# Kernel tuning notes

Measured on AMD Instinct MI355X. Metric: run time of the kernel, lower is better.

The kernel has to match this reference:

```python
import jax, jax.numpy as jnp
import numpy as np
from jax import lax

B, CIN, H, W = 32, 256, 28, 28
COUT, KS, KEXP = 256, 3, 4
HIDDEN = int(CIN * 0.25)  # ratio hard-coded to 0.25 in the module


def setup_inputs() -> dict:
    key = jax.random.key(0)
    k1, k2, k3, k4 = jax.random.split(key, 4)
    x = jax.random.normal(k1, (B, CIN, H, W), dtype=jnp.float32)
    # SE (InvertedEx) params: fc1 (1x1 conv, no bias), fc2 (1x1 conv, bias)
    fc1_w = jax.random.normal(k2, (HIDDEN, CIN), dtype=jnp.float32) * np.float32(np.sqrt(2.0 / CIN))
    fc2_w = jax.random.normal(k3, (KEXP * COUT, HIDDEN), dtype=jnp.float32) * np.float32(np.sqrt(2.0 / HIDDEN))
    fc2_b = jnp.zeros((KEXP * COUT,), dtype=jnp.float32)
    # K expert conv kernels, he_std = sqrt(2) * (CIN*KS^2)^-0.5
    he_std = np.float32(np.sqrt(2.0) * (CIN * KS * KS) ** -0.5)
    weight = jax.random.normal(k4, (KEXP, COUT, CIN, KS, KS), dtype=jnp.float32) * he_std
    return {"x": x, "fc1_w": fc1_w, "fc2_w": fc2_w, "fc2_b": fc2_b, "weight": weight}


def reference(x, fc1_w, fc2_w, fc2_b, weight):
    # --- SE routing ---
    pooled = jnp.mean(x, axis=(2, 3))                        # [B, CIN]
    h = jax.nn.relu(pooled @ fc1_w.T)                        # [B, HIDDEN]
    y = (h @ fc2_w.T + fc2_b).reshape(B, KEXP, COUT)         # [B, K, COUT]
    prob = jax.nn.softmax(y / jnp.sqrt(jnp.float32(HIDDEN)), axis=1)  # softmax over K
    # --- aggregate per-sample kernels ---
    agg_w = jnp.einsum('bko,koihw->boihw', prob, weight)     # [B, COUT, CIN, KS, KS]
    # --- per-sample conv (batched implicit GEMM via vmap) ---
    def conv1(xi, wi):
        return lax.conv_general_dilated(
            xi[None], wi, window_strides=(1, 1), padding=((1, 1), (1, 1)),
            dimension_numbers=('NCHW', 'OIHW', 'NCHW'))[0]
    out = jax.vmap(conv1)(x, agg_w)                          # [B, COUT, H, W]
    return out
```

## Files before the change

### kernel.cpp

```cpp
#include <hip/hip_runtime.h>
#include <math.h>

#define B_    32
#define CIN_  256
#define HW_   784
#define H_    28
#define W_    28
#define COUT_ 256
#define KEXP_ 4
#define HID_  64

typedef short short8 __attribute__((ext_vector_type(8)));
typedef float floatx16 __attribute__((ext_vector_type(16)));

__device__ __forceinline__ unsigned short f2bf(float f) {
    union { float f; unsigned int u; } v; v.f = f;
    unsigned int r = (v.u + 0x7FFFu + ((v.u >> 16) & 1u)) >> 16;
    return (unsigned short)r;
}

__global__ __launch_bounds__(256) void xpose_pool_kernel(const float* __restrict__ x,
                                                         unsigned short* __restrict__ x_t,
                                                         float* __restrict__ pooled) {
    __shared__ float tile[32][33];
    int bid = blockIdx.x;
    int b   = bid / 200;
    int rem = bid - b * 200;
    int ic0 = (rem / 25) * 32;
    int px0 = (rem % 25) * 32;
    int t = threadIdx.x;
    int c = t & 31, rr = t >> 5;
    #pragma unroll
    for (int r = 0; r < 4; ++r) {
        int icr = rr + r * 8;
        int px = px0 + c;
        float v = (px < HW_) ? x[((size_t)(b * CIN_ + ic0 + icr)) * HW_ + px] : 0.f;
        tile[icr][c] = v;
    }
    __syncthreads();
    #pragma unroll
    for (int r = 0; r < 4; ++r) {
        int pxr = rr + r * 8;
        int px = px0 + pxr;
        if (px < HW_)
            x_t[((size_t)b * HW_ + px) * CIN_ + ic0 + c] = f2bf(tile[c][pxr]);
    }
    if (t < 32) {
        float s = 0.f;
        #pragma unroll
        for (int cc = 0; cc < 32; ++cc) s += tile[t][cc];
        atomicAdd(&pooled[b * CIN_ + ic0 + t], s * (1.0f / HW_));
    }
}

__global__ __launch_bounds__(256) void pool_kernel(const float* __restrict__ x,
                                                   float* __restrict__ pooled) {
    int w = blockIdx.x * 4 + (threadIdx.x >> 6);
    int lane = threadIdx.x & 63;
    const float* p = x + (size_t)w * HW_;
    float s = 0.f;
    for (int i = lane; i < HW_; i += 64) s += p[i];
    for (int off = 32; off; off >>= 1) s += __shfl_down(s, off);
    if (lane == 0) pooled[w] = s * (1.0f / HW_);
}

__global__ __launch_bounds__(256) void se2_kernel(const float* __restrict__ pooled,
                                                  const float* __restrict__ fc1_w,
                                                  const float* __restrict__ fc2_w,
                                                  const float* __restrict__ fc2_b,
                                                  float* __restrict__ prob) {
    __shared__ float pl[CIN_];
    __shared__ float h[HID_];
    __shared__ float wb[16640];
    int b = blockIdx.x, t = threadIdx.x;
    pl[t] = pooled[b * CIN_ + t];
    #pragma unroll
    for (int i = 0; i < 16; ++i) {
        int l = t + i * 256;
        float4 v = *(const float4*)(fc1_w + (size_t)l * 4);
        int r = l >> 6, cc = (l & 63) * 4;
        float* dst = &wb[r * 257 + cc];
        dst[0] = v.x; dst[1] = v.y; dst[2] = v.z; dst[3] = v.w;
    }
    __syncthreads();
    if (t < HID_) {
        float s = 0.f;
        const float* wr = &wb[t * 257];
        for (int c = 0; c < CIN_; ++c) s += pl[c] * wr[c];
        h[t] = fmaxf(s, 0.f);
    }
    float yk[KEXP_];
    for (int k = 0; k < KEXP_; ++k) {
        __syncthreads();
        #pragma unroll
        for (int i = 0; i < 16; ++i) {
            int l = t + i * 256;
            float4 v = *(const float4*)(fc2_w + (size_t)k * COUT_ * HID_ + (size_t)l * 4);
            int o = l >> 4, jj = (l & 15) * 4;
            float* dst = &wb[o * 65 + jj];
            dst[0] = v.x; dst[1] = v.y; dst[2] = v.z; dst[3] = v.w;
        }
        __syncthreads();
        float s = fc2_b[k * COUT_ + t];
        const float* wr = &wb[t * 65];
        #pragma unroll
        for (int j = 0; j < HID_; ++j) s += h[j] * wr[j];
        yk[k] = s * 0.125f;
    }
    float m = yk[0];
    for (int k = 1; k < KEXP_; ++k) m = fmaxf(m, yk[k]);
    float e[KEXP_], sum = 0.f;
    for (int k = 0; k < KEXP_; ++k) { e[k] = expf(yk[k] - m); sum += e[k]; }
    float inv = 1.0f / sum;
    for (int k = 0; k < KEXP_; ++k)
        prob[b * (KEXP_ * COUT_) + k * COUT_ + t] = e[k] * inv;
}

__global__ __launch_bounds__(256) void agg2_kernel(const float* __restrict__ weight,
                                                   const float* __restrict__ prob,
                                                   unsigned short* __restrict__ agg) {
    __shared__ float ws_w[KEXP_ * CIN_ * 9];
    __shared__ float pb[KEXP_][8];
    int bid = blockIdx.x;
    int oc = bid & 255;
    int b0 = (bid >> 8) * 8;
    int t = threadIdx.x;
    for (int e = t; e < KEXP_ * CIN_ * 9; e += 256) {
        int k = e / (CIN_ * 9);
        int r = e - k * (CIN_ * 9);
        ws_w[e] = weight[((size_t)(k * COUT_ + oc)) * (CIN_ * 9) + r];
    }
    if (t < KEXP_ * 8) {
        int k = t >> 3, bb = t & 7;
        pb[k][bb] = prob[(b0 + bb) * (KEXP_ * COUT_) + k * COUT_ + oc];
    }
    __syncthreads();
    int ic = t;
    for (int rs = 0; rs < 9; ++rs) {
        float w0 = ws_w[0 * CIN_ * 9 + ic * 9 + rs];
        float w1 = ws_w[1 * CIN_ * 9 + ic * 9 + rs];
        float w2 = ws_w[2 * CIN_ * 9 + ic * 9 + rs];
        float w3 = ws_w[3 * CIN_ * 9 + ic * 9 + rs];
        #pragma unroll
        for (int bb = 0; bb < 8; ++bb) {
            float s = pb[0][bb] * w0 + pb[1][bb] * w1 + pb[2][bb] * w2 + pb[3][bb] * w3;
            agg[(((size_t)(b0 + bb) * 9 + rs) * COUT_ + oc) * CIN_ + ic] = f2bf(s);
        }
    }
}

__global__ __launch_bounds__(256, 2) void conv_mfma2_kernel(const unsigned short* __restrict__ x_t,
                                                            const unsigned short* __restrict__ agg,
                                                            float* __restrict__ out) {
    __shared__ __align__(16) short Xs[6 * 35 * 72];
    __shared__ __align__(16) short As[2][128 * 72];

    int gid = blockIdx.x;
    int rowblk = gid >> 6;
    int pair = gid & 63;
    int b = pair >> 1;
    int oc0 = (pair & 1) * 128;
    int py0 = rowblk * 4;

    int t = threadIdx.x;
    int lane = t & 63, w = t >> 6;
    int ml = lane & 31, kh = lane >> 5;

    floatx16 acc[4];
    #pragma unroll
    for (int j = 0; j < 4; ++j)
        #pragma unroll
        for (int r = 0; r < 16; ++r) acc[j][r] = 0.f;

    const unsigned short* xtb = x_t + (size_t)b * HW_ * CIN_;
    const unsigned short* agb = agg + ((size_t)b * 9 * COUT_ + oc0) * CIN_;

    int arow = t >> 3, ag = t & 7;

    for (int ic0 = 0; ic0 < CIN_; ic0 += 64) {
        #pragma unroll
        for (int i = 0; i < 7; ++i) {
            int l = t + i * 256;
            if (l < 6 * 35 * 8) {
                int pos = l >> 3, g = l & 7;
                int row = pos / 35, col = pos - row * 35;
                int gy = py0 - 1 + row, gx = col - 1;
                short8 v = (short8)0;
                if ((unsigned)gy < 28u && (unsigned)gx < 28u)
                    v = *(const short8*)(xtb + ((size_t)(gy * W_ + gx)) * CIN_ + ic0 + g * 8);
                *(short8*)&Xs[pos * 72 + g * 8] = v;
            }
        }
        {
            const unsigned short* ap = agb + ic0 + (size_t)ag * 8;
            #pragma unroll
            for (int i = 0; i < 4; ++i) {
                short8 v = *(const short8*)(ap + (size_t)(arow + i * 32) * CIN_);
                *(short8*)&As[0][(arow + i * 32) * 72 + ag * 8] = v;
            }
        }
        __syncthreads();

        for (int rs = 0; rs < 9; ++rs) {
            int cur = rs & 1;
            int dy = rs / 3, dx = rs - dy * 3;
            short8 rv0, rv1, rv2, rv3;
            if (rs < 8) {
                const unsigned short* ap = agb + (size_t)(rs + 1) * COUT_ * CIN_ + ic0 + (size_t)ag * 8;
                rv0 = *(const short8*)(ap + (size_t)(arow +  0) * CIN_);
                rv1 = *(const short8*)(ap + (size_t)(arow + 32) * CIN_);
                rv2 = *(const short8*)(ap + (size_t)(arow + 64) * CIN_);
                rv3 = *(const short8*)(ap + (size_t)(arow + 96) * CIN_);
            }
            #pragma unroll
            for (int kk = 0; kk < 4; ++kk) {
                short8 a = *(const short8*)&As[cur][(w * 32 + ml) * 72 + kk * 16 + kh * 8];
                #pragma unroll
                for (int j = 0; j < 4; ++j) {
                    short8 bf = *(const short8*)&Xs[((j + dy) * 35 + (ml + dx)) * 72 + kk * 16 + kh * 8];
                    acc[j] = __builtin_amdgcn_mfma_f32_32x32x16_bf16(a, bf, acc[j], 0, 0, 0);
                }
            }
            if (rs < 8) {
                short* dst = &As[cur ^ 1][arow * 72 + ag * 8];
                *(short8*)(dst +  0 * 72)      = rv0;
                *(short8*)(dst + 32 * 72)      = rv1;
                *(short8*)(dst + 64 * 72)      = rv2;
                *(short8*)(dst + 96 * 72)      = rv3;
            }
            __syncthreads();
        }
    }

    int col = ml;
    if (col < W_) {
        #pragma unroll
        for (int j = 0; j < 4; ++j) {
            int y = py0 + j;
            #pragma unroll
            for (int r = 0; r < 16; ++r) {
                int ocg = oc0 + w * 32 + (r & 3) + 8 * (r >> 2) + 4 * kh;
                out[((size_t)(b * COUT_ + ocg)) * HW_ + y * W_ + col] = acc[j][r];
            }
        }
    }
}

__global__ __launch_bounds__(256) void conv_kernel(const float* __restrict__ x,
                                                   const float* __restrict__ weight,
                                                   const float* __restrict__ prob,
                                                   float* __restrict__ out) {
    __shared__ float xs[30 * 30];
    __shared__ float wagg[8][32][12];
    __shared__ float pl[KEXP_][8];

    int b  = blockIdx.x >> 5;
    int o0 = (blockIdx.x & 31) * 8;
    int t  = threadIdx.x;

    if (t < 32) {
        int k = t >> 3, oc = t & 7;
        pl[k][oc] = prob[b * (KEXP_ * COUT_) + k * COUT_ + o0 + oc];
    }
    int p0 = t;
    int pr[4], pc[4];
    bool pv[4];
    #pragma unroll
    for (int j = 0; j < 4; ++j) {
        int p = p0 + j * 256;
        pv[j] = p < HW_;
        pr[j] = p / W_;
        pc[j] = p % W_;
    }
    float acc[8][4];
    #pragma unroll
    for (int oc = 0; oc < 8; ++oc)
        #pragma unroll
        for (int j = 0; j < 4; ++j) acc[oc][j] = 0.f;

    int aoc = t >> 5, aii = t & 31;

    for (int ic0 = 0; ic0 < CIN_; ic0 += 32) {
        __syncthreads();
        {
            float w9[9];
            #pragma unroll
            for (int j = 0; j < 9; ++j) w9[j] = 0.f;
            int i = ic0 + aii;
            #pragma unroll
            for (int k = 0; k < KEXP_; ++k) {
                float pk = pl[k][aoc];
                const float* wp = weight + ((size_t)(k * COUT_ + o0 + aoc) * CIN_ + i) * 9;
                #pragma unroll
                for (int j = 0; j < 9; ++j) w9[j] += pk * wp[j];
            }
            #pragma unroll
            for (int j = 0; j < 9; ++j) wagg[aoc][aii][j] = w9[j];
        }
        for (int ii = 0; ii < 32; ++ii) {
            int i = ic0 + ii;
            __syncthreads();
            const float* xp = x + (size_t)(b * CIN_ + i) * HW_;
            for (int e = t; e < 900; e += 256) {
                int ry = e / 30, cx = e - ry * 30;
                int gy = ry - 1, gx = cx - 1;
                float v = 0.f;
                if ((unsigned)gy < 28u && (unsigned)gx < 28u) v = xp[gy * W_ + gx];
                xs[e] = v;
            }
            __syncthreads();
            float xv[4][9];
            #pragma unroll
            for (int j = 0; j < 4; ++j) {
                if (pv[j]) {
                    const float* xr = &xs[pr[j] * 30 + pc[j]];
                    xv[j][0] = xr[0];  xv[j][1] = xr[1];  xv[j][2] = xr[2];
                    xv[j][3] = xr[30]; xv[j][4] = xr[31]; xv[j][5] = xr[32];
                    xv[j][6] = xr[60]; xv[j][7] = xr[61]; xv[j][8] = xr[62];
                } else {
                    #pragma unroll
                    for (int q = 0; q < 9; ++q) xv[j][q] = 0.f;
                }
            }
            #pragma unroll
            for (int oc = 0; oc < 8; ++oc) {
                float4 wa = *(const float4*)&wagg[oc][ii][0];
                float4 wb2 = *(const float4*)&wagg[oc][ii][4];
                float  wc = wagg[oc][ii][8];
                #pragma unroll
                for (int j = 0; j < 4; ++j) {
                    acc[oc][j] += xv[j][0] * wa.x + xv[j][1] * wa.y + xv[j][2] * wa.z
                                + xv[j][3] * wa.w + xv[j][4] * wb2.x + xv[j][5] * wb2.y
                                + xv[j][6] * wb2.z + xv[j][7] * wb2.w + xv[j][8] * wc;
                }
            }
        }
    }
    #pragma unroll
    for (int oc = 0; oc < 8; ++oc) {
        float* op = out + (size_t)(b * COUT_ + o0 + oc) * HW_ + p0;
        #pragma unroll
        for (int j = 0; j < 4; ++j)
            if (pv[j]) op[j * 256] = acc[oc][j];
    }
}

extern "C" void kernel_launch(void* const* d_in, const int* in_sizes, int n_in,
                              void* d_out, int out_size, void* d_ws, size_t ws_size,
                              hipStream_t stream) {
    const float* x     = (const float*)d_in[0];
    const float* fc1_w = (const float*)d_in[1];
    const float* fc2_w = (const float*)d_in[2];
    const float* fc2_b = (const float*)d_in[3];
    const float* weight= (const float*)d_in[4];
    float* out = (float*)d_out;

    char* ws = (char*)d_ws;
    float* pooled = (float*)(ws);
    float* prob   = (float*)(ws + 32768);
    unsigned short* x_t = (unsigned short*)(ws + 163840);
    unsigned short* agg = (unsigned short*)(ws + 13008896);
    const size_t WS_NEED = 50757632;

    if (ws_size >= WS_NEED) {
        hipMemsetAsync(pooled, 0, B_ * CIN_ * sizeof(float), stream);
        xpose_pool_kernel<<<B_ * 8 * 25, 256, 0, stream>>>(x, x_t, pooled);
        se2_kernel<<<B_, 256, 0, stream>>>(pooled, fc1_w, fc2_w, fc2_b, prob);
        agg2_kernel<<<4 * COUT_, 256, 0, stream>>>(weight, prob, agg);
        conv_mfma2_kernel<<<7 * 64, 256, 0, stream>>>(x_t, agg, out);
    } else {
        pool_kernel<<<(B_ * CIN_) / 4, 256, 0, stream>>>(x, pooled);
        se2_kernel<<<B_, 256, 0, stream>>>(pooled, fc1_w, fc2_w, fc2_b, prob);
        conv_kernel<<<B_ * (COUT_ / 8), 256, 0, stream>>>(x, weight, prob, out);
    }
}
```

Before: 156.8 us.

## Rework dynamic-conv pipeline: partial pooling, vectorized aggregation, register-streamed conv tiles

Swaps the pooled atomics and memset for per-tile partial sums that the SE kernel reduces itself, so one launch and the atomic traffic go away. Vectorizes the weight aggregation with float4 loads and packed 4-wide bf16 stores. Rewrites the MFMA conv to compute 7 output rows per block, with each A fragment reused across three row offsets. A fragments are prefetched straight from global into registers rather than staged in LDS, and X is double-buffered across input-channel chunks. Launching 256 blocks at one block per CU leaves occupancy low and raises register pressure, and the partial buffer aliases the agg region.

```diff
diff --git a/kernel.cpp b/kernel.cpp
--- a/kernel.cpp
+++ b/kernel.cpp
@@ -11,6 +11,7 @@
 #define HID_  64
 
 typedef short short8 __attribute__((ext_vector_type(8)));
+typedef unsigned short ushort4v __attribute__((ext_vector_type(4)));
 typedef float floatx16 __attribute__((ext_vector_type(16)));
 
 __device__ __forceinline__ unsigned short f2bf(float f) {
@@ -21,13 +22,15 @@
 
 __global__ __launch_bounds__(256) void xpose_pool_kernel(const float* __restrict__ x,
                                                          unsigned short* __restrict__ x_t,
-                                                         float* __restrict__ pooled) {
+                                                         float* __restrict__ partial) {
     __shared__ float tile[32][33];
     int bid = blockIdx.x;
     int b   = bid / 200;
     int rem = bid - b * 200;
-    int ic0 = (rem / 25) * 32;
-    int px0 = (rem % 25) * 32;
+    int icg = rem / 25;
+    int pxt = rem % 25;
+    int ic0 = icg * 32;
+    int px0 = pxt * 32;
     int t = threadIdx.x;
     int c = t & 31, rr = t >> 5;
     #pragma unroll
@@ -49,7 +52,7 @@
         float s = 0.f;
         #pragma unroll
         for (int cc = 0; cc < 32; ++cc) s += tile[t][cc];
-        atomicAdd(&pooled[b * CIN_ + ic0 + t], s * (1.0f / HW_));
+        partial[((size_t)b * 25 + pxt) * CIN_ + ic0 + t] = s * (1.0f / HW_);
     }
 }
 
@@ -62,6 +65,63 @@
     for (int i = lane; i < HW_; i += 64) s += p[i];
     for (int off = 32; off; off >>= 1) s += __shfl_down(s, off);
     if (lane == 0) pooled[w] = s * (1.0f / HW_);
+}
+
+__global__ __launch_bounds__(256) void se3_kernel(const float* __restrict__ partial,
+                                                  const float* __restrict__ fc1_w,
+                                                  const float* __restrict__ fc2_w,
+                                                  const float* __restrict__ fc2_b,
+                                                  float* __restrict__ prob) {
+    __shared__ float pl[CIN_];
+    __shared__ float h[HID_];
+    __shared__ float wb[16640];
+    int b = blockIdx.x, t = threadIdx.x;
+    {
+        float s = 0.f;
+        for (int pt = 0; pt < 25; ++pt)
+            s += partial[((size_t)b * 25 + pt) * CIN_ + t];
+        pl[t] = s;
+    }
+    #pragma unroll
+    for (int i = 0; i < 16; ++i) {
+        int l = t + i * 256;
+        float4 v = *(const float4*)(fc1_w + (size_t)l * 4);
+        int r = l >> 6, cc = (l & 63) * 4;
+        float* dst = &wb[r * 257 + cc];
+        dst[0] = v.x; dst[1] = v.y; dst[2] = v.z; dst[3] = v.w;
+    }
+    __syncthreads();
+    if (t < HID_) {
+        float s = 0.f;
+        const float* wr = &wb[t * 257];
+        for (int c = 0; c < CIN_; ++c) s += pl[c] * wr[c];
+        h[t] = fmaxf(s, 0.f);
+    }
+    float yk[KEXP_];
+    for (int k = 0; k < KEXP_; ++k) {
+        __syncthreads();
+        #pragma unroll
+        for (int i = 0; i < 16; ++i) {
+            int l = t + i * 256;
+            float4 v = *(const float4*)(fc2_w + (size_t)k * COUT_ * HID_ + (size_t)l * 4);
+            int o = l >> 4, jj = (l & 15) * 4;
+            float* dst = &wb[o * 65 + jj];
+            dst[0] = v.x; dst[1] = v.y; dst[2] = v.z; dst[3] = v.w;
+        }
+        __syncthreads();
+        float s = fc2_b[k * COUT_ + t];
+        const float* wr = &wb[t * 65];
+        #pragma unroll
+        for (int j = 0; j < HID_; ++j) s += h[j] * wr[j];
+        yk[k] = s * 0.125f;
+    }
+    float m = yk[0];
+    for (int k = 1; k < KEXP_; ++k) m = fmaxf(m, yk[k]);
+    float e[KEXP_], sum = 0.f;
+    for (int k = 0; k < KEXP_; ++k) { e[k] = expf(yk[k] - m); sum += e[k]; }
+    float inv = 1.0f / sum;
+    for (int k = 0; k < KEXP_; ++k)
+        prob[b * (KEXP_ * COUT_) + k * COUT_ + t] = e[k] * inv;
 }
 
 __global__ __launch_bounds__(256) void se2_kernel(const float* __restrict__ pooled,
@@ -116,7 +176,7 @@
         prob[b * (KEXP_ * COUT_) + k * COUT_ + t] = e[k] * inv;
 }
 
-__global__ __launch_bounds__(256) void agg2_kernel(const float* __restrict__ weight,
+__global__ __launch_bounds__(256) void agg3_kernel(const float* __restrict__ weight,
                                                    const float* __restrict__ prob,
                                                    unsigned short* __restrict__ agg) {
     __shared__ float ws_w[KEXP_ * CIN_ * 9];
@@ -125,122 +185,158 @@
     int oc = bid & 255;
     int b0 = (bid >> 8) * 8;
     int t = threadIdx.x;
-    for (int e = t; e < KEXP_ * CIN_ * 9; e += 256) {
-        int k = e / (CIN_ * 9);
-        int r = e - k * (CIN_ * 9);
-        ws_w[e] = weight[((size_t)(k * COUT_ + oc)) * (CIN_ * 9) + r];
+    #pragma unroll
+    for (int i = 0; i < 9; ++i) {
+        int e4 = t + i * 256;
+        int k = e4 / 576;
+        int r4 = e4 - k * 576;
+        float4 v = *(const float4*)(weight + (size_t)k * 589824 + (size_t)oc * 2304 + (size_t)r4 * 4);
+        *(float4*)&ws_w[e4 * 4] = v;
     }
     if (t < KEXP_ * 8) {
         int k = t >> 3, bb = t & 7;
-        pb[k][bb] = prob[(b0 + bb) * (KEXP_ * COUT_) + k * COUT_ + oc];
+        pb[k][bb] = prob[(size_t)(b0 + bb) * (KEXP_ * COUT_) + k * COUT_ + oc];
     }
     __syncthreads();
-    int ic = t;
+    int icg = t & 63, blane = t >> 6;
     for (int rs = 0; rs < 9; ++rs) {
-        float w0 = ws_w[0 * CIN_ * 9 + ic * 9 + rs];
-        float w1 = ws_w[1 * CIN_ * 9 + ic * 9 + rs];
-        float w2 = ws_w[2 * CIN_ * 9 + ic * 9 + rs];
-        float w3 = ws_w[3 * CIN_ * 9 + ic * 9 + rs];
-        #pragma unroll
-        for (int bb = 0; bb < 8; ++bb) {
-            float s = pb[0][bb] * w0 + pb[1][bb] * w1 + pb[2][bb] * w2 + pb[3][bb] * w3;
-            agg[(((size_t)(b0 + bb) * 9 + rs) * COUT_ + oc) * CIN_ + ic] = f2bf(s);
-        }
-    }
-}
-
-__global__ __launch_bounds__(256, 2) void conv_mfma2_kernel(const unsigned short* __restrict__ x_t,
+        float wv[4][4];
+        #pragma unroll
+        for (int q = 0; q < 4; ++q)
+            #pragma unroll
+            for (int k = 0; k < 4; ++k)
+                wv[q][k] = ws_w[k * 2304 + (icg * 4 + q) * 9 + rs];
+        #pragma unroll
+        for (int bb = 0; bb < 2; ++bb) {
+            int bidx = blane * 2 + bb;
+            float p0 = pb[0][bidx], p1 = pb[1][bidx], p2 = pb[2][bidx], p3 = pb[3][bidx];
+            ushort4v pack;
+            #pragma unroll
+            for (int q = 0; q < 4; ++q) {
+                float s = p0 * wv[q][0] + p1 * wv[q][1] + p2 * wv[q][2] + p3 * wv[q][3];
+                pack[q] = f2bf(s);
+            }
+            *(ushort4v*)(agg + ((((size_t)(b0 + bidx) * 9 + rs) * COUT_ + oc)) * CIN_ + icg * 4) = pack;
+        }
+    }
+}
+
+__global__ __launch_bounds__(256, 1) void conv_mfma3_kernel(const unsigned short* __restrict__ x_t,
                                                             const unsigned short* __restrict__ agg,
                                                             float* __restrict__ out) {
-    __shared__ __align__(16) short Xs[6 * 35 * 72];
-    __shared__ __align__(16) short As[2][128 * 72];
+    __shared__ __align__(16) short Xs[2][9 * 35 * 72];
 
     int gid = blockIdx.x;
+    int b      = gid & 31;
+    int oc0    = ((gid >> 5) & 1) * 128;
     int rowblk = gid >> 6;
-    int pair = gid & 63;
-    int b = pair >> 1;
-    int oc0 = (pair & 1) * 128;
-    int py0 = rowblk * 4;
+    int py0 = rowblk * 7;
 
     int t = threadIdx.x;
     int lane = t & 63, w = t >> 6;
     int ml = lane & 31, kh = lane >> 5;
 
-    floatx16 acc[4];
-    #pragma unroll
-    for (int j = 0; j < 4; ++j)
+    floatx16 acc[7];
+    #pragma unroll
+    for (int j = 0; j < 7; ++j)
         #pragma unroll
         for (int r = 0; r < 16; ++r) acc[j][r] = 0.f;
 
     const unsigned short* xtb = x_t + (size_t)b * HW_ * CIN_;
-    const unsigned short* agb = agg + ((size_t)b * 9 * COUT_ + oc0) * CIN_;
-
-    int arow = t >> 3, ag = t & 7;
-
-    for (int ic0 = 0; ic0 < CIN_; ic0 += 64) {
-        #pragma unroll
-        for (int i = 0; i < 7; ++i) {
+    const unsigned short* aln = agg + (((size_t)b * 9 * COUT_) + oc0 + w * 32 + ml) * CIN_ + kh * 8;
+
+    {
+        #pragma unroll
+        for (int i = 0; i < 10; ++i) {
             int l = t + i * 256;
-            if (l < 6 * 35 * 8) {
+            if (l < 2520) {
                 int pos = l >> 3, g = l & 7;
                 int row = pos / 35, col = pos - row * 35;
                 int gy = py0 - 1 + row, gx = col - 1;
                 short8 v = (short8)0;
                 if ((unsigned)gy < 28u && (unsigned)gx < 28u)
-                    v = *(const short8*)(xtb + ((size_t)(gy * W_ + gx)) * CIN_ + ic0 + g * 8);
-                *(short8*)&Xs[pos * 72 + g * 8] = v;
-            }
-        }
-        {
-            const unsigned short* ap = agb + ic0 + (size_t)ag * 8;
-            #pragma unroll
-            for (int i = 0; i < 4; ++i) {
-                short8 v = *(const short8*)(ap + (size_t)(arow + i * 32) * CIN_);
-                *(short8*)&As[0][(arow + i * 32) * 72 + ag * 8] = v;
-            }
-        }
-        __syncthreads();
-
-        for (int rs = 0; rs < 9; ++rs) {
-            int cur = rs & 1;
-            int dy = rs / 3, dx = rs - dy * 3;
-            short8 rv0, rv1, rv2, rv3;
-            if (rs < 8) {
-                const unsigned short* ap = agb + (size_t)(rs + 1) * COUT_ * CIN_ + ic0 + (size_t)ag * 8;
-                rv0 = *(const short8*)(ap + (size_t)(arow +  0) * CIN_);
-                rv1 = *(const short8*)(ap + (size_t)(arow + 32) * CIN_);
-                rv2 = *(const short8*)(ap + (size_t)(arow + 64) * CIN_);
-                rv3 = *(const short8*)(ap + (size_t)(arow + 96) * CIN_);
-            }
-            #pragma unroll
-            for (int kk = 0; kk < 4; ++kk) {
-                short8 a = *(const short8*)&As[cur][(w * 32 + ml) * 72 + kk * 16 + kh * 8];
+                    v = *(const short8*)(xtb + ((size_t)(gy * W_ + gx)) * CIN_ + g * 8);
+                *(short8*)&Xs[0][pos * 72 + g * 8] = v;
+            }
+        }
+    }
+
+    short8 Acur0, Acur1, Acur2, Anext0, Anext1, Anext2;
+    Acur0 = *(const short8*)(aln + (size_t)(0 * 3 + 0) * (COUT_ * CIN_));
+    Acur1 = *(const short8*)(aln + (size_t)(1 * 3 + 0) * (COUT_ * CIN_));
+    Acur2 = *(const short8*)(aln + (size_t)(2 * 3 + 0) * (COUT_ * CIN_));
+    int dxn = 1, kkn = 0, icn = 0;
+
+    __syncthreads();
+
+    for (int c = 0; c < 4; ++c) {
+        int ic0 = c * 64;
+        const short* xb = &Xs[c & 1][0];
+
+        short8 Xl[10];
+        if (c < 3) {
+            #pragma unroll
+            for (int i = 0; i < 10; ++i) {
+                int l = t + i * 256;
+                short8 v = (short8)0;
+                if (l < 2520) {
+                    int pos = l >> 3, g = l & 7;
+                    int row = pos / 35, col = pos - row * 35;
+                    int gy = py0 - 1 + row, gx = col - 1;
+                    if ((unsigned)gy < 28u && (unsigned)gx < 28u)
+                        v = *(const short8*)(xtb + ((size_t)(gy * W_ + gx)) * CIN_ + ic0 + 64 + g * 8);
+                }
+                Xl[i] = v;
+            }
+        }
+
+        for (int kk = 0; kk < 4; ++kk) {
+            for (int dx = 0; dx < 3; ++dx) {
+                if (icn < 256) {
+                    const unsigned short* ap = aln + icn + kkn * 16;
+                    Anext0 = *(const short8*)(ap + (size_t)(0 * 3 + dxn) * (COUT_ * CIN_));
+                    Anext1 = *(const short8*)(ap + (size_t)(1 * 3 + dxn) * (COUT_ * CIN_));
+                    Anext2 = *(const short8*)(ap + (size_t)(2 * 3 + dxn) * (COUT_ * CIN_));
+                    ++dxn;
+                    if (dxn == 3) { dxn = 0; ++kkn; if (kkn == 4) { kkn = 0; icn += 64; } }
+                }
+                int va = (ml + dx) * 72 + kk * 16 + kh * 8;
                 #pragma unroll
-                for (int j = 0; j < 4; ++j) {
-                    short8 bf = *(const short8*)&Xs[((j + dy) * 35 + (ml + dx)) * 72 + kk * 16 + kh * 8];
-                    acc[j] = __builtin_amdgcn_mfma_f32_32x32x16_bf16(a, bf, acc[j], 0, 0, 0);
-                }
-            }
-            if (rs < 8) {
-                short* dst = &As[cur ^ 1][arow * 72 + ag * 8];
-                *(short8*)(dst +  0 * 72)      = rv0;
-                *(short8*)(dst + 32 * 72)      = rv1;
-                *(short8*)(dst + 64 * 72)      = rv2;
-                *(short8*)(dst + 96 * 72)      = rv3;
-            }
-            __syncthreads();
-        }
-    }
-
-    int col = ml;
-    if (col < W_) {
-        #pragma unroll
-        for (int j = 0; j < 4; ++j) {
-            int y = py0 + j;
+                for (int r = 0; r < 9; ++r) {
+                    short8 Bf = *(const short8*)&xb[r * 2520 + va];
+                    if (r <= 6)
+                        acc[r]     = __builtin_amdgcn_mfma_f32_32x32x16_bf16(Acur0, Bf, acc[r], 0, 0, 0);
+                    if (r >= 1 && r - 1 <= 6)
+                        acc[r - 1] = __builtin_amdgcn_mfma_f32_32x32x16_bf16(Acur1, Bf, acc[r - 1], 0, 0, 0);
+                    if (r >= 2)
+                        acc[r - 2] = __builtin_amdgcn_mfma_f32_32x32x16_bf16(Acur2, Bf, acc[r - 2], 0, 0, 0);
+                }
+                Acur0 = Anext0; Acur1 = Anext1; Acur2 = Anext2;
+            }
+        }
+
+        if (c < 3) {
+            short* dstb = &Xs[(c & 1) ^ 1][0];
+            #pragma unroll
+            for (int i = 0; i < 10; ++i) {
+                int l = t + i * 256;
+                if (l < 2520) {
+                    int pos = l >> 3, g = l & 7;
+                    *(short8*)&dstb[pos * 72 + g * 8] = Xl[i];
+                }
+            }
+        }
+        __syncthreads();
+    }
+
+    if (ml < W_) {
+        #pragma unroll
+        for (int j = 0; j < 7; ++j) {
+            float* op = out + ((size_t)(b * COUT_ + oc0 + w * 32)) * HW_ + (py0 + j) * W_ + ml;
             #pragma unroll
             for (int r = 0; r < 16; ++r) {
-                int ocg = oc0 + w * 32 + (r & 3) + 8 * (r >> 2) + 4 * kh;
-                out[((size_t)(b * COUT_ + ocg)) * HW_ + y * W_ + col] = acc[j][r];
+                int ocd = (r & 3) + 8 * (r >> 2) + 4 * kh;
+                op[(size_t)ocd * HW_] = acc[j][r];
             }
         }
     }
@@ -356,19 +452,19 @@
     float* out = (float*)d_out;
 
     char* ws = (char*)d_ws;
-    float* pooled = (float*)(ws);
-    float* prob   = (float*)(ws + 32768);
-    unsigned short* x_t = (unsigned short*)(ws + 163840);
-    unsigned short* agg = (unsigned short*)(ws + 13008896);
-    const size_t WS_NEED = 50757632;
+    float* prob = (float*)(ws);
+    unsigned short* x_t = (unsigned short*)(ws + 131072);
+    unsigned short* agg = (unsigned short*)(ws + 12976128);
+    float* partial = (float*)(ws + 12976128);
+    const size_t WS_NEED = 12976128 + (size_t)B_ * 9 * COUT_ * CIN_ * 2;
 
     if (ws_size >= WS_NEED) {
-        hipMemsetAsync(pooled, 0, B_ * CIN_ * sizeof(float), stream);
-        xpose_pool_kernel<<<B_ * 8 * 25, 256, 0, stream>>>(x, x_t, pooled);
-        se2_kernel<<<B_, 256, 0, stream>>>(pooled, fc1_w, fc2_w, fc2_b, prob);
-        agg2_kernel<<<4 * COUT_, 256, 0, stream>>>(weight, prob, agg);
-        conv_mfma2_kernel<<<7 * 64, 256, 0, stream>>>(x_t, agg, out);
+        xpose_pool_kernel<<<B_ * 8 * 25, 256, 0, stream>>>(x, x_t, partial);
+        se3_kernel<<<B_, 256, 0, stream>>>(partial, fc1_w, fc2_w, fc2_b, prob);
+        agg3_kernel<<<4 * COUT_, 256, 0, stream>>>(weight, prob, agg);
+        conv_mfma3_kernel<<<256, 256, 0, stream>>>(x_t, agg, out);
     } else {
+        float* pooled = (float*)(ws + 131072);
         pool_kernel<<<(B_ * CIN_) / 4, 256, 0, stream>>>(x, pooled);
         se2_kernel<<<B_, 256, 0, stream>>>(pooled, fc1_w, fc2_w, fc2_b, prob);
         conv_kernel<<<B_ * (COUT_ / 8), 256, 0, stream>>>(x, weight, prob, out);
```

Result: faster. 149.9 us (-4.4%).
